# Kernel tuning notes

Hardware: AMD Instinct MI355X
Metric: run time of the kernel (lower is better)

Reference implementation:

```python
import jax, jax.numpy as jnp
from jax import lax
import numpy as np

GAMMA = 0.1           # softmin temperature (init kwarg gamma)
NORMALIZE = True      # init kwarg normalize
BIG = jnp.float32(1e30)  # stand-in for DBL_MAX boundary (finite to keep grads NaN-free)


def _sq_dist(x, y):
    # x: [b, m, d], y: [b, n, d] -> [b, m, n] squared euclidean distances
    return jnp.sum((x[:, :, None, :] - y[:, None, :, :]) ** 2, axis=-1)


def _softmin3(a, b, c):
    # -gamma * log(exp(-a/g) + exp(-b/g) + exp(-c/g)), numerically stable
    z = jnp.stack([a, b, c], axis=0) * (-1.0 / GAMMA)
    return -GAMMA * jax.nn.logsumexp(z, axis=0)


def _soft_dtw(D):
    # D: [m, n] cost matrix -> scalar soft-DTW value R[m, n]
    m, n = D.shape
    # R row 0: R[0,0]=0, R[0,j]=BIG for j>=1
    init_row = jnp.concatenate([jnp.zeros((1,), D.dtype), jnp.full((n,), BIG, D.dtype)])

    def row_step(prev_row, d_row):
        # prev_row = R[i-1, 0..n]; d_row = D[i-1, 0..n-1]
        up = prev_row[1:]       # R[i-1, j]
        upleft = prev_row[:-1]  # R[i-1, j-1]

        def col_step(left, inp):
            d, u, ul = inp
            r = d + _softmin3(u, ul, left)
            return r, r

        _, row_vals = lax.scan(col_step, BIG, (d_row, up, upleft))
        new_row = jnp.concatenate([jnp.full((1,), BIG, D.dtype), row_vals])
        return new_row, None

    last_row, _ = lax.scan(row_step, init_row, D)
    return last_row[-1]


_soft_dtw_batch = jax.vmap(_soft_dtw)  # [b, m, n] -> [b]


def setup_inputs() -> dict:
    key = jax.random.key(0)
    kx, ky = jax.random.split(key)
    x = jax.random.normal(kx, (64, 256, 8), dtype=jnp.float32)
    y = jax.random.normal(ky, (64, 256, 8), dtype=jnp.float32)
    return {"x": x, "y": y}


def reference(x, y):
    loss_xy = _soft_dtw_batch(_sq_dist(x, y))
    if NORMALIZE:
        loss_xx = _soft_dtw_batch(_sq_dist(x, x))
        loss_yy = _soft_dtw_batch(_sq_dist(y, y))
        total = loss_xy - 0.5 * (loss_xx + loss_yy)
    else:
        total = loss_xy
    return jnp.mean(total)
```

## Files before the change

### kernel.cpp

```cpp
#include <hip/hip_runtime.h>

static constexpr float K1   = -14.426950408889634074f;
static constexpr float KOUT = -0.069314718055994530942f;
static constexpr float WBIG = -1.0e30f;

__device__ __forceinline__ float dpp_shr1(float v, float fill) {
    int r = __builtin_amdgcn_update_dpp(__float_as_int(fill), __float_as_int(v),
                                        0x138 , 0xf, 0xf, false);
    return __int_as_float(r);
}

__global__ void __launch_bounds__(64, 1)
sdtw_kernel(const float* __restrict__ x, const float* __restrict__ y,
            float* __restrict__ out)
{
    const int batch = blockIdx.x;
    const int pair  = blockIdx.y;
    const int lane  = threadIdx.x;

    const float* A  = (pair == 2 ? y : x) + batch * 2048;
    const float* Bp = (pair == 1 ? x : y) + batch * 2048;

    __shared__ float xT[9][256];

    #pragma unroll
    for (int rr = 0; rr < 4; ++rr) {
        int r = lane + rr * 64;
        float4 a0 = *reinterpret_cast<const float4*>(A + r * 8);
        float4 a1 = *reinterpret_cast<const float4*>(A + r * 8 + 4);
        xT[0][r] = a0.x; xT[1][r] = a0.y; xT[2][r] = a0.z; xT[3][r] = a0.w;
        xT[4][r] = a1.x; xT[5][r] = a1.y; xT[6][r] = a1.z; xT[7][r] = a1.w;
        xT[8][r] = a0.x*a0.x + a0.y*a0.y + a0.z*a0.z + a0.w*a0.w
                 + a1.x*a1.x + a1.y*a1.y + a1.z*a1.z + a1.w*a1.w;
    }

    float b[4][8], nb[4];
    #pragma unroll
    for (int cc = 0; cc < 4; ++cc) {
        const float* bp = Bp + (4 * lane + cc) * 8;
        float4 b0 = *reinterpret_cast<const float4*>(bp);
        float4 b1 = *reinterpret_cast<const float4*>(bp + 4);
        b[cc][0]=b0.x; b[cc][1]=b0.y; b[cc][2]=b0.z; b[cc][3]=b0.w;
        b[cc][4]=b1.x; b[cc][5]=b1.y; b[cc][6]=b1.z; b[cc][7]=b1.w;
        nb[cc] = b0.x*b0.x + b0.y*b0.y + b0.z*b0.z + b0.w*b0.w
               + b1.x*b1.x + b1.y*b1.y + b1.z*b1.z + b1.w*b1.w;
    }

    __syncthreads();

    float up[4];
    up[0]=up[1]=up[2]=up[3] = WBIG;
    float own_last  = WBIG;
    float left_prev = (lane == 0) ? 0.0f : WBIG;

    float xa[9], xb[9];
    #pragma unroll
    for (int d = 0; d < 9; ++d) xa[d] = xT[d][0];

    auto step = [&](int s, float (&xc)[9], float (&xn)[9]) {
        int ipf = s + 1 - lane;
        ipf = ipf < 0 ? 0 : (ipf > 255 ? 255 : ipf);
        #pragma unroll
        for (int d = 0; d < 9; ++d) xn[d] = xT[d][ipf];

        float lin  = dpp_shr1(own_last, WBIG);
        float ulin = left_prev;
        left_prev  = lin;

        const int i = s - lane;
        if (i >= 0 && i < 256) {
            float u0 = up[0], u1 = up[1], u2 = up[2], u3 = up[3];
            float ul0 = ulin;
            if (i == 0) {
                u0 = u1 = u2 = u3 = WBIG;
                if (lane != 0) ul0 = WBIG;
            }
            const float uu [4] = { u0, u1, u2, u3 };
            const float uls[4] = { ul0, u0, u1, u2 };

            float m2[4], p2[4];
            #pragma unroll
            for (int cc = 0; cc < 4; ++cc) {
                float d2 = uu[cc] - uls[cc];
                m2[cc] = fmaxf(uu[cc], uls[cc]);
                p2[cc] = 1.0f + __builtin_amdgcn_exp2f(fminf(d2, 0.0f - d2));
            }

            float Dw[4];
            #pragma unroll
            for (int cc = 0; cc < 4; ++cc) {
                float acc = xc[0] * b[cc][0];
                #pragma unroll
                for (int d = 1; d < 8; ++d) acc = fmaf(xc[d], b[cc][d], acc);
                Dw[cc] = fmaf(-2.0f, acc, xc[8] + nb[cc]) * K1;
            }

            float lft = lin;
            #pragma unroll
            for (int cc = 0; cc < 4; ++cc) {
                float m   = fmaxf(m2[cc], lft);
                float ea  = __builtin_amdgcn_exp2f(lft - m);
                float eb  = __builtin_amdgcn_exp2f(m2[cc] - m);
                float sum = fmaf(p2[cc], eb, ea);
                float w   = (Dw[cc] + m) + __builtin_amdgcn_logf(sum);
                up[cc] = w;
                lft    = w;
            }
            own_last = lft;
        }
    };

    for (int s = 0; s < 320; s += 2) {
        step(s,     xa, xb);
        step(s + 1, xb, xa);
    }

    if (lane == 63) {
        float r   = own_last * KOUT;
        float wgt = (pair == 0) ? (1.0f / 64.0f) : (-0.5f / 64.0f);
        atomicAdd(out, r * wgt);
    }
}

extern "C" void kernel_launch(void* const* d_in, const int* in_sizes, int n_in,
                              void* d_out, int out_size, void* d_ws, size_t ws_size,
                              hipStream_t stream)
{
    const float* x = (const float*)d_in[0];
    const float* y = (const float*)d_in[1];
    float* out = (float*)d_out;

    hipMemsetAsync(out, 0, out_size * sizeof(float), stream);
    hipLaunchKernelGGL(sdtw_kernel, dim3(64, 3), dim3(64), 0, stream, x, y, out);
}
```

Measured before the change: 148.6 us.

## Use fp16 dot2 distances, log-add-exp softmin chain, and phase-split wavefront loop

Stores x in shared memory as packed fp16 pairs and computes distances and norms with fdot2 instead of fp32 FMAs, which shrinks LDS traffic and ALU work per step. The three-way softmin is rewritten as two nested pairwise log-add-exp operations, so the serial dependency chain through the left neighbour is shorter (max, exp2, log, add). The wavefront loop is split into ramp-up, steady and drain phases so the steady phase drops the boundary checks. Using fp16 inputs loses precision in the distance values and may change the result beyond tolerance.

```diff
diff --git a/kernel.cpp b/kernel.cpp
--- a/kernel.cpp
+++ b/kernel.cpp
@@ -1,6 +1,10 @@
 #include <hip/hip_runtime.h>
+#include <type_traits>
+
+typedef _Float16 h2 __attribute__((ext_vector_type(2)));
 
 static constexpr float K1   = -14.426950408889634074f;
+static constexpr float M2K1 = 28.853900817779268148f;
 static constexpr float KOUT = -0.069314718055994530942f;
 static constexpr float WBIG = -1.0e30f;
 
@@ -10,7 +14,20 @@
     return __int_as_float(r);
 }
 
-__global__ void __launch_bounds__(64, 1)
+__device__ __forceinline__ unsigned pack2(float a, float b) {
+    h2 p; p[0] = (_Float16)a; p[1] = (_Float16)b;
+    return __builtin_bit_cast(unsigned, p);
+}
+
+__device__ __forceinline__ float hdot(h2 a, h2 b, float c) {
+#if __has_builtin(__builtin_amdgcn_fdot2)
+    return __builtin_amdgcn_fdot2(a, b, c, false);
+#else
+    return fmaf((float)a[1], (float)b[1], fmaf((float)a[0], (float)b[0], c));
+#endif
+}
+
+__global__ void __attribute__((amdgpu_waves_per_eu(1, 1))) __launch_bounds__(64, 1)
 sdtw_kernel(const float* __restrict__ x, const float* __restrict__ y,
             float* __restrict__ out)
 {
@@ -21,88 +38,98 @@
     const float* A  = (pair == 2 ? y : x) + batch * 2048;
     const float* Bp = (pair == 1 ? x : y) + batch * 2048;
 
-    __shared__ float xT[9][256];
+    __shared__ unsigned xHs[4][256];
+    __shared__ float    nxs[256];
 
     #pragma unroll
     for (int rr = 0; rr < 4; ++rr) {
         int r = lane + rr * 64;
         float4 a0 = *reinterpret_cast<const float4*>(A + r * 8);
         float4 a1 = *reinterpret_cast<const float4*>(A + r * 8 + 4);
-        xT[0][r] = a0.x; xT[1][r] = a0.y; xT[2][r] = a0.z; xT[3][r] = a0.w;
-        xT[4][r] = a1.x; xT[5][r] = a1.y; xT[6][r] = a1.z; xT[7][r] = a1.w;
-        xT[8][r] = a0.x*a0.x + a0.y*a0.y + a0.z*a0.z + a0.w*a0.w
-                 + a1.x*a1.x + a1.y*a1.y + a1.z*a1.z + a1.w*a1.w;
+        unsigned u0 = pack2(a0.x, a0.y), u1 = pack2(a0.z, a0.w);
+        unsigned u2 = pack2(a1.x, a1.y), u3 = pack2(a1.z, a1.w);
+        xHs[0][r] = u0; xHs[1][r] = u1; xHs[2][r] = u2; xHs[3][r] = u3;
+        h2 h0 = __builtin_bit_cast(h2, u0), h1 = __builtin_bit_cast(h2, u1);
+        h2 h2v = __builtin_bit_cast(h2, u2), h3 = __builtin_bit_cast(h2, u3);
+        nxs[r] = hdot(h3, h3, hdot(h2v, h2v, hdot(h1, h1, hdot(h0, h0, 0.0f))));
     }
 
-    float b[4][8], nb[4];
+    h2 bh[4][4]; float Knb[4];
     #pragma unroll
     for (int cc = 0; cc < 4; ++cc) {
         const float* bp = Bp + (4 * lane + cc) * 8;
         float4 b0 = *reinterpret_cast<const float4*>(bp);
         float4 b1 = *reinterpret_cast<const float4*>(bp + 4);
-        b[cc][0]=b0.x; b[cc][1]=b0.y; b[cc][2]=b0.z; b[cc][3]=b0.w;
-        b[cc][4]=b1.x; b[cc][5]=b1.y; b[cc][6]=b1.z; b[cc][7]=b1.w;
-        nb[cc] = b0.x*b0.x + b0.y*b0.y + b0.z*b0.z + b0.w*b0.w
-               + b1.x*b1.x + b1.y*b1.y + b1.z*b1.z + b1.w*b1.w;
+        bh[cc][0] = __builtin_bit_cast(h2, pack2(b0.x, b0.y));
+        bh[cc][1] = __builtin_bit_cast(h2, pack2(b0.z, b0.w));
+        bh[cc][2] = __builtin_bit_cast(h2, pack2(b1.x, b1.y));
+        bh[cc][3] = __builtin_bit_cast(h2, pack2(b1.z, b1.w));
+        float nb = hdot(bh[cc][3], bh[cc][3], hdot(bh[cc][2], bh[cc][2],
+                   hdot(bh[cc][1], bh[cc][1], hdot(bh[cc][0], bh[cc][0], 0.0f))));
+        Knb[cc] = K1 * nb;
     }
 
     __syncthreads();
 
-    float up[4];
-    up[0]=up[1]=up[2]=up[3] = WBIG;
+    float up[4] = {WBIG, WBIG, WBIG, WBIG};
     float own_last  = WBIG;
     float left_prev = (lane == 0) ? 0.0f : WBIG;
 
-    float xa[9], xb[9];
-    #pragma unroll
-    for (int d = 0; d < 9; ++d) xa[d] = xT[d][0];
+    unsigned xc[4], xn[4]; float nxc, nxn;
+    xc[0]=xHs[0][0]; xc[1]=xHs[1][0]; xc[2]=xHs[2][0]; xc[3]=xHs[3][0]; nxc=nxs[0];
 
-    auto step = [&](int s, float (&xc)[9], float (&xn)[9]) {
+    auto step = [&](auto phc, int s, unsigned (&XC)[4], float& NXC,
+                    unsigned (&XN)[4], float& NXN) {
+        constexpr int PH = decltype(phc)::value;
         int ipf = s + 1 - lane;
         ipf = ipf < 0 ? 0 : (ipf > 255 ? 255 : ipf);
-        #pragma unroll
-        for (int d = 0; d < 9; ++d) xn[d] = xT[d][ipf];
+        XN[0]=xHs[0][ipf]; XN[1]=xHs[1][ipf]; XN[2]=xHs[2][ipf]; XN[3]=xHs[3][ipf];
+        NXN = nxs[ipf];
 
         float lin  = dpp_shr1(own_last, WBIG);
         float ulin = left_prev;
         left_prev  = lin;
 
         const int i = s - lane;
-        if (i >= 0 && i < 256) {
-            float u0 = up[0], u1 = up[1], u2 = up[2], u3 = up[3];
-            float ul0 = ulin;
-            if (i == 0) {
-                u0 = u1 = u2 = u3 = WBIG;
-                if (lane != 0) ul0 = WBIG;
+        bool act = (PH == 0) ? (i >= 0) : (PH == 2) ? (i < 256) : true;
+        if (act) {
+            float u0=up[0], u1=up[1], u2=up[2], u3=up[3];
+            float ulc = ulin;
+            if (PH == 0) {
+                if (i == 0) { u0=u1=u2=u3=WBIG; if (lane) ulc = WBIG; }
             }
-            const float uu [4] = { u0, u1, u2, u3 };
-            const float uls[4] = { ul0, u0, u1, u2 };
+            const float uu [4] = {u0, u1, u2, u3};
+            const float uls[4] = {ulc, u0, u1, u2};
 
-            float m2[4], p2[4];
+            float knx = K1 * NXC;
+            float Dw[4], a2[4], Dwa2[4];
+            h2 xv0 = __builtin_bit_cast(h2, XC[0]);
+            h2 xv1 = __builtin_bit_cast(h2, XC[1]);
+            h2 xv2 = __builtin_bit_cast(h2, XC[2]);
+            h2 xv3 = __builtin_bit_cast(h2, XC[3]);
+            #pragma unroll
+            for (int cc = 0; cc < 4; ++cc) {
+                float dot = hdot(xv3, bh[cc][3], hdot(xv2, bh[cc][2],
+                            hdot(xv1, bh[cc][1], hdot(xv0, bh[cc][0], 0.0f))));
+                Dw[cc] = fmaf(M2K1, dot, knx + Knb[cc]);
+            }
             #pragma unroll
             for (int cc = 0; cc < 4; ++cc) {
                 float d2 = uu[cc] - uls[cc];
-                m2[cc] = fmaxf(uu[cc], uls[cc]);
-                p2[cc] = 1.0f + __builtin_amdgcn_exp2f(fminf(d2, 0.0f - d2));
+                float m2 = fmaxf(uu[cc], uls[cc]);
+                float t  = __builtin_amdgcn_exp2f(-fabsf(d2));
+                float a  = m2 + __builtin_amdgcn_logf(1.0f + t);
+                a2[cc]   = a;
+                Dwa2[cc] = Dw[cc] + a;
             }
-
-            float Dw[4];
-            #pragma unroll
-            for (int cc = 0; cc < 4; ++cc) {
-                float acc = xc[0] * b[cc][0];
-                #pragma unroll
-                for (int d = 1; d < 8; ++d) acc = fmaf(xc[d], b[cc][d], acc);
-                Dw[cc] = fmaf(-2.0f, acc, xc[8] + nb[cc]) * K1;
-            }
-
             float lft = lin;
             #pragma unroll
             for (int cc = 0; cc < 4; ++cc) {
-                float m   = fmaxf(m2[cc], lft);
-                float ea  = __builtin_amdgcn_exp2f(lft - m);
-                float eb  = __builtin_amdgcn_exp2f(m2[cc] - m);
-                float sum = fmaf(p2[cc], eb, ea);
-                float w   = (Dw[cc] + m) + __builtin_amdgcn_logf(sum);
+                float q   = Dw[cc] + lft;
+                float dlt = a2[cc] - lft;
+                float t2  = __builtin_amdgcn_exp2f(-fabsf(dlt));
+                float l2  = __builtin_amdgcn_logf(1.0f + t2);
+                float w   = fmaxf(Dwa2[cc], q) + l2;
                 up[cc] = w;
                 lft    = w;
             }
@@ -110,10 +137,11 @@
         }
     };
 
-    for (int s = 0; s < 320; s += 2) {
-        step(s,     xa, xb);
-        step(s + 1, xb, xa);
-    }
+    std::integral_constant<int,0> P0; std::integral_constant<int,1> P1;
+    std::integral_constant<int,2> P2;
+    for (int s = 0;   s < 64;  s += 2) { step(P0, s, xc, nxc, xn, nxn); step(P0, s+1, xn, nxn, xc, nxc); }
+    for (int s = 64;  s < 256; s += 2) { step(P1, s, xc, nxc, xn, nxn); step(P1, s+1, xn, nxn, xc, nxc); }
+    for (int s = 256; s < 320; s += 2) { step(P2, s, xc, nxc, xn, nxn); step(P2, s+1, xn, nxn, xc, nxc); }
 
     if (lane == 63) {
         float r   = own_last * KOUT;
```

Result: faster. 126.0 us (-15.2%).
